# Optimization experiments

Measured on AMD Instinct MI355X. Metric: run time of the kernel, lower is better.

The kernel has to match this reference:

```python
import jax, jax.numpy as jnp
import numpy as np

B, T, C, L = 128, 512, 1024, 64
BLANK = C - 1          # keras ctc_batch_cost uses last class as blank
NEG = -1e9             # finite log-zero (grad-safe)
EPS = 1e-7             # keras.backend.epsilon()


def setup_inputs() -> dict:
    key = jax.random.key(0)
    k1, k2, k3, k4 = jax.random.split(key, 4)
    # y_pred: softmax probabilities, as ctc_batch_cost expects
    y_pred = jax.nn.softmax(jax.random.normal(k1, (B, T, C), dtype=jnp.float32), axis=-1)
    y_true = jax.random.randint(k2, (B, L), 0, BLANK).astype(jnp.int32)  # labels exclude blank
    input_length = jax.random.randint(k3, (B, 1), T // 2, T + 1).astype(jnp.int32)
    label_length = jax.random.randint(k4, (B, 1), L // 2, L + 1).astype(jnp.int32)
    return {"y_true": y_true, "y_pred": y_pred,
            "input_length": input_length, "label_length": label_length}


def _lse3(a, b, c):
    m = jnp.maximum(jnp.maximum(a, b), c)
    return m + jnp.log(jnp.exp(a - m) + jnp.exp(b - m) + jnp.exp(c - m))


def _ctc_loss(y_pred, y_true, input_length, label_length):
    # log probs, exactly as keras: log(y_pred + epsilon)
    logp = jnp.log(y_pred + EPS)                     # [B,T,C]
    Bsz, Tmax, _ = logp.shape
    Lm = y_true.shape[1]
    S = 2 * Lm + 1                                   # extended label length

    # extended labels: blank at even positions, labels at odd
    lab_ext = jnp.full((Bsz, S), BLANK, dtype=y_true.dtype).at[:, 1::2].set(y_true)
    s_idx = jnp.arange(S)
    in_len = input_length.reshape(-1)                # [B]
    lab_len = label_length.reshape(-1)               # [B]
    valid = s_idx[None, :] < (2 * lab_len[:, None] + 1)

    # skip transition s-2 -> s allowed iff lab[s] != blank and lab[s] != lab[s-2]
    lab_m2 = jnp.concatenate(
        [jnp.full((Bsz, 2), -1, dtype=lab_ext.dtype), lab_ext[:, :-2]], axis=1)
    skip_ok = (s_idx[None, :] >= 2) & (lab_ext != BLANK) & (lab_ext != lab_m2)

    # virtual alpha_{-1}: mass only at position 0
    alpha0 = jnp.broadcast_to(jnp.where(s_idx == 0, 0.0, NEG), (Bsz, S)).astype(logp.dtype)

    def step(alpha, inputs):
        lp_t, t = inputs                              # lp_t: [B,C]
        emit = jnp.take_along_axis(lp_t, lab_ext, axis=1)           # [B,S]
        s1 = jnp.concatenate([jnp.full((Bsz, 1), NEG, logp.dtype), alpha[:, :-1]], axis=1)
        s2 = jnp.concatenate([jnp.full((Bsz, 2), NEG, logp.dtype), alpha[:, :-2]], axis=1)
        s2 = jnp.where(skip_ok, s2, NEG)
        a = emit + _lse3(alpha, s1, s2)
        a = jnp.where(valid, a, NEG)
        # freeze alpha once t >= input_length (per-example variable T)
        a = jnp.where((t < in_len)[:, None], a, alpha)
        return a, None

    lp_tb = jnp.transpose(logp, (1, 0, 2))            # [T,B,C]
    alpha_T, _ = jax.lax.scan(step, alpha0, (lp_tb, jnp.arange(Tmax)))

    end_blank = 2 * lab_len                           # index of final blank
    end_label = 2 * lab_len - 1                       # index of final label
    a1 = jnp.take_along_axis(alpha_T, end_blank[:, None], axis=1)[:, 0]
    a2 = jnp.take_along_axis(alpha_T, end_label[:, None], axis=1)[:, 0]
    loss = -jnp.logaddexp(a1, a2)                     # [B]
    return loss[:, None]                              # keras returns [B,1]


def reference(y_true, y_pred, input_length, label_length):
    return _ctc_loss(y_pred, y_true, input_length, label_length)
```

## Files before the change

### kernel.cpp

```cpp
#include <hip/hip_runtime.h>


constexpr int Tmax   = 512;
constexpr int Cch    = 1024;
constexpr int Lm     = 64;
constexpr int BLANKC = Cch - 1;
constexpr int CH     = 64;
constexpr int NCH    = Tmax / CH;
constexpr int ROW    = 66;

#define NEGF (-1e9f)
#define EPSF (1e-7f)
#define LN2F (0.69314718055994530942f)

__device__ __forceinline__ float wave_shr1(float src, float fill) {
    int r = __builtin_amdgcn_update_dpp(__float_as_int(fill), __float_as_int(src),
                                        0x138, 0xf, 0xf, false);
    return __int_as_float(r);
}
__device__ __forceinline__ float lae2(float a, float b) {
    float m = fmaxf(a, b);
    return m + __builtin_log2f(__builtin_exp2f(a - m) + __builtin_exp2f(b - m));
}
__device__ __forceinline__ float lse3_2(float a, float b, float c) {
    float m = fmaxf(fmaxf(a, b), c);
    return m + __builtin_log2f(__builtin_exp2f(a - m) +
                               __builtin_exp2f(b - m) +
                               __builtin_exp2f(c - m));
}
__device__ __forceinline__ int clampi(int v, int lo, int hi) {
    return v < lo ? lo : (v > hi ? hi : v);
}

__global__ __launch_bounds__(1024, 1) void ctc_onekernel(
    const int*   __restrict__ y_true,
    const float* __restrict__ y_pred,
    const int*   __restrict__ in_len,
    const int*   __restrict__ lab_len,
    float*       __restrict__ out)
{
    const int b    = blockIdx.x;
    const int tid  = threadIdx.x;
    const int wave = tid >> 6;
    const int lane = tid & 63;

    __shared__ float Ebuf[2][CH * ROW];

    const int cls = y_true[b * Lm + lane];
    const int Tb  = clampi(in_len[b], 0, Tmax);
    const int lb  = clampi(lab_len[b], 0, Lm);
    const float* __restrict__ base = y_pred + (size_t)b * Tmax * Cch;

    auto gather = [&](int c) {
        const int tbase = c * CH;
        const int tt0   = wave - 1;
        float pc[5], pb[5];
#pragma unroll
        for (int k = 0; k < 5; ++k) {
            const int tt = tt0 + 15 * k;
            if (tt < CH) {
                const float* row = base + (size_t)(tbase + tt) * Cch;
                pc[k] = row[cls];
                pb[k] = row[BLANKC];
            }
        }
#pragma unroll
        for (int k = 0; k < 5; ++k) {
            const int tt = tt0 + 15 * k;
            if (tt < CH) {
                float* dst = &Ebuf[c & 1][tt * ROW];
                dst[lane] = __builtin_log2f(pc[k] + EPSF);
                if (lane == 0) dst[64] = __builtin_log2f(pb[k] + EPSF);
            }
        }
    };

    const int  cls_prev = __shfl_up(cls, 1, 64);
    const bool skip     = (lane >= 1) && (cls != cls_prev);
    const bool val_lo   = (lane <= lb);
    const bool val_hi   = (lane <  lb);
    const bool val_ex   = (lb == Lm);

    float a_lo = (lane == 0) ? 0.f : NEGF;
    float a_hi = NEGF;
    float a_ex = NEGF;

    if (wave != 0) gather(0);
    __syncthreads();

    for (int c = 0; c < NCH; ++c) {
        if (wave == 0) {
            const int tbase = c * CH;
            if (tbase < Tb) {
                const int steps = (Tb - tbase) < CH ? (Tb - tbase) : CH;
                const float* eb = Ebuf[c & 1];
                float rc[4], rb[4];
#pragma unroll
                for (int i = 0; i < 4; ++i) {
                    rc[i] = eb[i * ROW + lane];
                    rb[i] = eb[i * ROW + 64];
                }
                for (int i0 = 0; i0 < CH; i0 += 4) {
#pragma unroll
                    for (int j = 0; j < 4; ++j) {
                        const int i = i0 + j;
                        if (i >= steps) break;
                        const float e_c = rc[j];
                        const float e_b = rb[j];
                        const int tn = i + 4;
                        if (tn < CH) {
                            rc[j] = eb[tn * ROW + lane];
                            rb[j] = eb[tn * ROW + 64];
                        }
                        const float p_hi = wave_shr1(a_hi, NEGF);
                        float n_lo = e_b + lae2(a_lo, p_hi);
                        float n_hi = e_c + lse3_2(a_hi, a_lo, skip ? p_hi : NEGF);
                        float n_ex = e_b + lae2(a_ex, a_hi);
                        a_lo = val_lo ? n_lo : NEGF;
                        a_hi = val_hi ? n_hi : NEGF;
                        a_ex = val_ex ? n_ex : NEGF;
                    }
                    if (i0 + 4 >= steps) break;
                }
            }
        } else {
            if (c + 1 < NCH && (c + 1) * CH < Tb) gather(c + 1);
        }
        __syncthreads();
    }

    if (wave == 0) {
        const float a_end_blank = (lb == Lm) ? __shfl(a_ex, 63, 64)
                                             : __shfl(a_lo, lb, 64);
        const int   el_lane     = (lb >= 1) ? (lb - 1) : 0;
        const float a_end_label = (lb >= 1) ? __shfl(a_hi, el_lane, 64)
                                            : __shfl(a_lo, 0, 64);
        if (lane == 0) {
            out[b] = -LN2F * lae2(a_end_blank, a_end_label);
        }
    }
}

extern "C" void kernel_launch(void* const* d_in, const int* in_sizes, int n_in,
                              void* d_out, int out_size, void* d_ws, size_t ws_size,
                              hipStream_t stream) {
    const int*   y_true  = (const int*)  d_in[0];
    const float* y_pred  = (const float*)d_in[1];
    const int*   in_len  = (const int*)  d_in[2];
    const int*   lab_len = (const int*)  d_in[3];
    float*       out     = (float*)      d_out;

    ctc_onekernel<<<dim3(128), dim3(1024), 0, stream>>>(
        y_true, y_pred, in_len, lab_len, out);
}
```

Before: 416.5 us.

## Split CTC input gather across helper blocks via cooperative grid sync

Launches 256 cooperative blocks of 512 threads instead of 128 blocks of 1024. The second half are helper blocks that pre-gather and log-transform the emission rows for the later time chunks into a global scratch buffer. A grid-wide sync makes them visible, and owner blocks then copy those chunks from scratch into shared memory instead of doing strided HBM gathers. The goal is to overlap the latency-bound gather with the serial recursion using more CUs. The cost is a grid sync, an extra global round trip, and a dependence on cooperative launch residency.

```diff
diff --git a/kernel.cpp b/kernel.cpp
--- a/kernel.cpp
+++ b/kernel.cpp
@@ -1,4 +1,7 @@
 #include <hip/hip_runtime.h>
+#include <hip/hip_cooperative_groups.h>
+
+namespace cg = cooperative_groups;
 
 
 constexpr int Tmax   = 512;
@@ -7,11 +10,16 @@
 constexpr int BLANKC = Cch - 1;
 constexpr int CH     = 64;
 constexpr int NCH    = Tmax / CH;
+constexpr int SPLIT  = 4;
 constexpr int ROW    = 66;
+constexpr int NB     = 128;
+constexpr int EROWS  = Tmax - SPLIT * CH;
 
 #define NEGF (-1e9f)
 #define EPSF (1e-7f)
 #define LN2F (0.69314718055994530942f)
+
+__device__ float gE[(size_t)NB * EROWS * ROW];
 
 __device__ __forceinline__ float wave_shr1(float src, float fill) {
     int r = __builtin_amdgcn_update_dpp(__float_as_int(fill), __float_as_int(src),
@@ -32,47 +40,90 @@
     return v < lo ? lo : (v > hi ? hi : v);
 }
 
-__global__ __launch_bounds__(1024, 1) void ctc_onekernel(
+__global__ __launch_bounds__(512, 1) void ctc_coop(
     const int*   __restrict__ y_true,
     const float* __restrict__ y_pred,
     const int*   __restrict__ in_len,
     const int*   __restrict__ lab_len,
     float*       __restrict__ out)
 {
-    const int b    = blockIdx.x;
-    const int tid  = threadIdx.x;
-    const int wave = tid >> 6;
-    const int lane = tid & 63;
+    const int  bid   = blockIdx.x;
+    const bool owner = bid < NB;
+    const int  b     = owner ? bid : bid - NB;
+    const int  tid   = threadIdx.x;
+    const int  wave  = tid >> 6;
+    const int  lane  = tid & 63;
 
     __shared__ float Ebuf[2][CH * ROW];
 
     const int cls = y_true[b * Lm + lane];
     const int Tb  = clampi(in_len[b], 0, Tmax);
-    const int lb  = clampi(lab_len[b], 0, Lm);
     const float* __restrict__ base = y_pred + (size_t)b * Tmax * Cch;
 
-    auto gather = [&](int c) {
+    cg::grid_group grid = cg::this_grid();
+
+    if (!owner) {
+        for (int c = SPLIT; c < NCH; ++c) {
+            const int tbase = c * CH;
+            if (tbase >= Tb) break;
+            float pc[8], pb[8];
+#pragma unroll
+            for (int k = 0; k < 8; ++k) {
+                const int tt = wave + 8 * k;
+                if (tbase + tt < Tb) {
+                    const float* row = base + (size_t)(tbase + tt) * Cch;
+                    pc[k] = row[cls];
+                    pb[k] = row[BLANKC];
+                }
+            }
+            float* dstc = gE + ((size_t)b * EROWS + (size_t)(c - SPLIT) * CH) * ROW;
+#pragma unroll
+            for (int k = 0; k < 8; ++k) {
+                const int tt = wave + 8 * k;
+                if (tbase + tt < Tb) {
+                    float* dst = dstc + tt * ROW;
+                    dst[lane] = __builtin_log2f(pc[k] + EPSF);
+                    if (lane == 0) dst[64] = __builtin_log2f(pb[k] + EPSF);
+                }
+            }
+        }
+        __threadfence();
+        grid.sync();
+        return;
+    }
+
+    const int lb = clampi(lab_len[b], 0, Lm);
+
+    auto gather_hbm = [&](int c) {
         const int tbase = c * CH;
         const int tt0   = wave - 1;
-        float pc[5], pb[5];
-#pragma unroll
-        for (int k = 0; k < 5; ++k) {
-            const int tt = tt0 + 15 * k;
+        float pc[10], pb[10];
+#pragma unroll
+        for (int k = 0; k < 10; ++k) {
+            const int tt = tt0 + 7 * k;
             if (tt < CH) {
                 const float* row = base + (size_t)(tbase + tt) * Cch;
                 pc[k] = row[cls];
                 pb[k] = row[BLANKC];
             }
         }
-#pragma unroll
-        for (int k = 0; k < 5; ++k) {
-            const int tt = tt0 + 15 * k;
+        float* dst0 = Ebuf[c & 1];
+#pragma unroll
+        for (int k = 0; k < 10; ++k) {
+            const int tt = tt0 + 7 * k;
             if (tt < CH) {
-                float* dst = &Ebuf[c & 1][tt * ROW];
+                float* dst = dst0 + tt * ROW;
                 dst[lane] = __builtin_log2f(pc[k] + EPSF);
                 if (lane == 0) dst[64] = __builtin_log2f(pb[k] + EPSF);
             }
         }
+    };
+
+    auto copy_E = [&](int c) {
+        const float* src = gE + ((size_t)b * EROWS + (size_t)(c - SPLIT) * CH) * ROW;
+        float* dst = Ebuf[c & 1];
+        for (int i = tid - 64; i < CH * ROW; i += 448)
+            dst[i] = src[i];
     };
 
     const int  cls_prev = __shfl_up(cls, 1, 64);
@@ -85,10 +136,11 @@
     float a_hi = NEGF;
     float a_ex = NEGF;
 
-    if (wave != 0) gather(0);
+    if (wave != 0) gather_hbm(0);
     __syncthreads();
 
     for (int c = 0; c < NCH; ++c) {
+        if (c == SPLIT - 1) grid.sync();
         if (wave == 0) {
             const int tbase = c * CH;
             if (tbase < Tb) {
@@ -124,7 +176,11 @@
                 }
             }
         } else {
-            if (c + 1 < NCH && (c + 1) * CH < Tb) gather(c + 1);
+            const int n = c + 1;
+            if (n < NCH && n * CH < Tb) {
+                if (n < SPLIT) gather_hbm(n);
+                else           copy_E(n);
+            }
         }
         __syncthreads();
     }
@@ -150,6 +206,8 @@
     const int*   lab_len = (const int*)  d_in[3];
     float*       out     = (float*)      d_out;
 
-    ctc_onekernel<<<dim3(128), dim3(1024), 0, stream>>>(
-        y_true, y_pred, in_len, lab_len, out);
-}
+    void* args[] = {(void*)&y_true, (void*)&y_pred, (void*)&in_len,
+                    (void*)&lab_len, (void*)&out};
+    hipLaunchCooperativeKernel((void*)ctc_coop, dim3(2 * NB), dim3(512),
+                               args, 0, stream);
+}
```

New measurement: 514.9 us. 23.6% more time.

## Split gather into a wide parallel pre-kernel and a lean recurrence kernel

Applied to the files above, without the earlier changes.

Moves the emission gather and log out of the per-batch recurrence kernel into a separate kernel launched over 2048 blocks. That kernel reads whole rows with coalesced float4 loads, stages them in LDS, and writes log2 emissions to a global scratch buffer. The recurrence kernel now only copies precomputed chunks from global into LDS with 512 threads. The aim is to take the latency-bound scattered gather off the 128-block serial path and use the whole GPU's bandwidth for it. The cost is reading full rows (all of y_pred) plus an extra global round trip and a second launch.

```diff
diff --git a/kernel.cpp b/kernel.cpp
--- a/kernel.cpp
+++ b/kernel.cpp
@@ -8,10 +8,14 @@
 constexpr int CH     = 64;
 constexpr int NCH    = Tmax / CH;
 constexpr int ROW    = 66;
+constexpr int NB     = 128;
+constexpr int RPB    = 32;
 
 #define NEGF (-1e9f)
 #define EPSF (1e-7f)
 #define LN2F (0.69314718055994530942f)
+
+__device__ __align__(16) float gE[(size_t)NB * Tmax * ROW];
 
 __device__ __forceinline__ float wave_shr1(float src, float fill) {
     int r = __builtin_amdgcn_update_dpp(__float_as_int(fill), __float_as_int(src),
@@ -32,12 +36,67 @@
     return v < lo ? lo : (v > hi ? hi : v);
 }
 
-__global__ __launch_bounds__(1024, 1) void ctc_onekernel(
+__global__ __launch_bounds__(256, 8) void ctc_gather(
     const int*   __restrict__ y_true,
     const float* __restrict__ y_pred,
-    const int*   __restrict__ in_len,
-    const int*   __restrict__ lab_len,
-    float*       __restrict__ out)
+    const int*   __restrict__ in_len)
+{
+    const int blk  = blockIdx.x;
+    const int b    = blk / (Tmax / RPB);
+    const int t0   = (blk % (Tmax / RPB)) * RPB;
+    const int tid  = threadIdx.x;
+    const int wave = tid >> 6;
+    const int lane = tid & 63;
+
+    const int Tb = clampi(in_len[b], 0, Tmax);
+    if (t0 >= Tb) return;
+
+    __shared__ float rowbuf[4][Cch];
+
+    const int cls = y_true[b * Lm + lane];
+    const float* __restrict__ base = y_pred + (size_t)b * Tmax * Cch;
+
+    constexpr int NK = RPB / 4;
+    float4 v0, v1, v2, v3;
+
+    auto issue = [&](int k) {
+        const int t = t0 + 4 * k + wave;
+        if (t < Tb) {
+            const float4* src = (const float4*)(base + (size_t)t * Cch);
+            v0 = src[lane];
+            v1 = src[64  + lane];
+            v2 = src[128 + lane];
+            v3 = src[192 + lane];
+        }
+    };
+
+    issue(0);
+    for (int k = 0; k < NK; ++k) {
+        const int t = t0 + 4 * k + wave;
+        const bool act = (t < Tb);
+        if (act) {
+            float4* lbuf = (float4*)rowbuf[wave];
+            lbuf[lane]        = v0;
+            lbuf[64  + lane]  = v1;
+            lbuf[128 + lane]  = v2;
+            lbuf[192 + lane]  = v3;
+        }
+        if (k + 1 < NK) issue(k + 1);
+        if (act) {
+            const float pc = rowbuf[wave][cls];
+            const float pb = rowbuf[wave][BLANKC];
+            float* dst = gE + ((size_t)b * Tmax + t) * ROW;
+            dst[lane] = __builtin_log2f(pc + EPSF);
+            if (lane == 0) dst[64] = __builtin_log2f(pb + EPSF);
+        }
+    }
+}
+
+__global__ __launch_bounds__(512, 1) void ctc_rec(
+    const int* __restrict__ y_true,
+    const int* __restrict__ in_len,
+    const int* __restrict__ lab_len,
+    float*     __restrict__ out)
 {
     const int b    = blockIdx.x;
     const int tid  = threadIdx.x;
@@ -49,30 +108,12 @@
     const int cls = y_true[b * Lm + lane];
     const int Tb  = clampi(in_len[b], 0, Tmax);
     const int lb  = clampi(lab_len[b], 0, Lm);
-    const float* __restrict__ base = y_pred + (size_t)b * Tmax * Cch;
 
-    auto gather = [&](int c) {
-        const int tbase = c * CH;
-        const int tt0   = wave - 1;
-        float pc[5], pb[5];
-#pragma unroll
-        for (int k = 0; k < 5; ++k) {
-            const int tt = tt0 + 15 * k;
-            if (tt < CH) {
-                const float* row = base + (size_t)(tbase + tt) * Cch;
-                pc[k] = row[cls];
-                pb[k] = row[BLANKC];
-            }
-        }
-#pragma unroll
-        for (int k = 0; k < 5; ++k) {
-            const int tt = tt0 + 15 * k;
-            if (tt < CH) {
-                float* dst = &Ebuf[c & 1][tt * ROW];
-                dst[lane] = __builtin_log2f(pc[k] + EPSF);
-                if (lane == 0) dst[64] = __builtin_log2f(pb[k] + EPSF);
-            }
-        }
+    auto copy_E = [&](int c) {
+        const float4* src = (const float4*)(gE + ((size_t)b * Tmax + c * CH) * ROW);
+        float4* dst = (float4*)Ebuf[c & 1];
+        for (int i = tid - 64; i < CH * ROW / 4; i += 448)
+            dst[i] = src[i];
     };
 
     const int  cls_prev = __shfl_up(cls, 1, 64);
@@ -85,7 +126,7 @@
     float a_hi = NEGF;
     float a_ex = NEGF;
 
-    if (wave != 0) gather(0);
+    if (wave != 0 && Tb > 0) copy_E(0);
     __syncthreads();
 
     for (int c = 0; c < NCH; ++c) {
@@ -124,7 +165,8 @@
                 }
             }
         } else {
-            if (c + 1 < NCH && (c + 1) * CH < Tb) gather(c + 1);
+            const int n = c + 1;
+            if (n < NCH && n * CH < Tb) copy_E(n);
         }
         __syncthreads();
     }
@@ -150,6 +192,8 @@
     const int*   lab_len = (const int*)  d_in[3];
     float*       out     = (float*)      d_out;
 
-    ctc_onekernel<<<dim3(128), dim3(1024), 0, stream>>>(
-        y_true, y_pred, in_len, lab_len, out);
+    ctc_gather<<<dim3(NB * (Tmax / RPB)), dim3(256), 0, stream>>>(
+        y_true, y_pred, in_len);
+    ctc_rec<<<dim3(NB), dim3(512), 0, stream>>>(
+        y_true, in_len, lab_len, out);
 }
```

Result: slower. 483.2 us (+16.0%).

## Stage full probability rows through LDS with coalesced float4 loads

Applied to the files above, without the earlier changes.

Gather waves now read whole 4KB rows of y_pred with coalesced float4 loads into a per-wave LDS staging buffer, then pick the label and blank entries from LDS, instead of issuing scattered per-lane loads. The block is halved to 512 threads (7 gather waves), and loads are double-buffered in registers across rows. The aim is to replace uncoalesced random gathers with streaming loads. The cost is reading the full row (far more bytes) and fewer gather waves.

```diff
diff --git a/kernel.cpp b/kernel.cpp
--- a/kernel.cpp
+++ b/kernel.cpp
@@ -8,6 +8,8 @@
 constexpr int CH     = 64;
 constexpr int NCH    = Tmax / CH;
 constexpr int ROW    = 66;
+constexpr int NB     = 128;
+constexpr int GW     = 7;
 
 #define NEGF (-1e9f)
 #define EPSF (1e-7f)
@@ -32,7 +34,9 @@
     return v < lo ? lo : (v > hi ? hi : v);
 }
 
-__global__ __launch_bounds__(1024, 1) void ctc_onekernel(
+struct R4 { float4 a, b, c, d; };
+
+__global__ __launch_bounds__(512, 1) void ctc_fused(
     const int*   __restrict__ y_true,
     const float* __restrict__ y_pred,
     const int*   __restrict__ in_len,
@@ -45,6 +49,7 @@
     const int lane = tid & 63;
 
     __shared__ float Ebuf[2][CH * ROW];
+    __shared__ float rowstage[GW][Cch];
 
     const int cls = y_true[b * Lm + lane];
     const int Tb  = clampi(in_len[b], 0, Tmax);
@@ -54,24 +59,48 @@
     auto gather = [&](int c) {
         const int tbase = c * CH;
         const int tt0   = wave - 1;
-        float pc[5], pb[5];
-#pragma unroll
-        for (int k = 0; k < 5; ++k) {
-            const int tt = tt0 + 15 * k;
+        float* lbuf = rowstage[wave - 1];
+        R4 va, vb;
+
+        auto ld = [&](R4& v, int k) {
+            const int tt = tt0 + GW * k;
             if (tt < CH) {
-                const float* row = base + (size_t)(tbase + tt) * Cch;
-                pc[k] = row[cls];
-                pb[k] = row[BLANKC];
+                const int t = tbase + tt;
+                if (t < Tb) {
+                    const float4* s = (const float4*)(base + (size_t)t * Cch);
+                    v.a = s[lane];
+                    v.b = s[64  + lane];
+                    v.c = s[128 + lane];
+                    v.d = s[192 + lane];
+                }
             }
-        }
-#pragma unroll
-        for (int k = 0; k < 5; ++k) {
-            const int tt = tt0 + 15 * k;
-            if (tt < CH) {
-                float* dst = &Ebuf[c & 1][tt * ROW];
-                dst[lane] = __builtin_log2f(pc[k] + EPSF);
-                if (lane == 0) dst[64] = __builtin_log2f(pb[k] + EPSF);
-            }
+        };
+        auto wr = [&](R4& v, int k) -> bool {
+            const int tt = tt0 + GW * k;
+            if (tt >= CH) return false;
+            const int t = tbase + tt;
+            if (t >= Tb) return false;
+            float4* lb4 = (float4*)lbuf;
+            lb4[lane]        = v.a;
+            lb4[64  + lane]  = v.b;
+            lb4[128 + lane]  = v.c;
+            lb4[192 + lane]  = v.d;
+            return true;
+        };
+        auto gr = [&](int k, bool act) {
+            if (!act) return;
+            const int tt = tt0 + GW * k;
+            const float pc = lbuf[cls];
+            const float pb = lbuf[BLANKC];
+            float* dst = &Ebuf[c & 1][tt * ROW];
+            dst[lane] = __builtin_log2f(pc + EPSF);
+            if (lane == 0) dst[64] = __builtin_log2f(pb + EPSF);
+        };
+
+        ld(va, 0);
+        for (int k = 0; k < 10; k += 2) {
+            bool a0 = wr(va, k);     ld(vb, k + 1);  gr(k,     a0);
+            bool a1 = wr(vb, k + 1); ld(va, k + 2);  gr(k + 1, a1);
         }
     };
 
@@ -124,7 +153,8 @@
                 }
             }
         } else {
-            if (c + 1 < NCH && (c + 1) * CH < Tb) gather(c + 1);
+            const int n = c + 1;
+            if (n < NCH && n * CH < Tb) gather(n);
         }
         __syncthreads();
     }
@@ -150,6 +180,6 @@
     const int*   lab_len = (const int*)  d_in[3];
     float*       out     = (float*)      d_out;
 
-    ctc_onekernel<<<dim3(128), dim3(1024), 0, stream>>>(
+    ctc_fused<<<dim3(NB), dim3(512), 0, stream>>>(
         y_true, y_pred, in_len, lab_len, out);
 }
```

Measured after the change: 449.0 us. 1.08x slower.
